# Optimization experiments

Measured on AMD Instinct MI355X. Metric: run time of the kernel, lower is better.

Reference implementation:

```python
import jax, jax.numpy as jnp
import numpy as np

N = 100000   # nodes
E = 3200000  # edges (avg degree 32)
IN = 256     # in_features
OUT = 256    # out_features
L = 4        # n_latent heads
D = OUT // L # per-head emb dim


def setup_inputs() -> dict:
    key = jax.random.key(0)
    ks = jax.random.split(key, 8)
    return {
        "x": jax.random.normal(ks[0], (N, IN), jnp.float32),
        "src": jax.random.randint(ks[1], (E,), 0, N, jnp.int32),
        "dst": jax.random.randint(ks[2], (E,), 0, N, jnp.int32),
        "W_lin": jax.random.normal(ks[3], (IN, OUT), jnp.float32) * (1.0 / np.sqrt(IN)),
        "b_lin": jnp.zeros((OUT,), jnp.float32),
        "att_w": jax.random.normal(ks[4], (L, 2 * OUT), jnp.float32) * (1.0 / np.sqrt(2 * OUT)),
        "att_b": jnp.zeros((L,), jnp.float32),
        "emb_w": jax.random.normal(ks[5], (IN, D), jnp.float32) * (1.0 / np.sqrt(IN)),
        "emb_b": jnp.zeros((D,), jnp.float32),
    }


def reference(x, src, dst, W_lin, b_lin, att_w, att_b, emb_w, emb_b):
    n = x.shape[0]
    h = x @ W_lin + b_lin              # [N, OUT]
    h_em = x @ emb_w + emb_b           # [N, D]
    out_dim = h.shape[1]
    # concat-linear att(cat(h[src], h[dst])) decomposed into separable per-node scores
    a_src = att_w[:, :out_dim]         # [L, OUT]
    a_dst = att_w[:, out_dim:]         # [L, OUT]
    s_src = h @ a_src.T                # [N, L]
    s_dst = h @ a_dst.T                # [N, L]
    # per-edge sigmoid score for all latent heads at once
    e_ob = jax.nn.sigmoid(s_src[src] + s_dst[dst] + att_b)  # [E, L]
    # sparse softmax over edges grouped by source node (FactorGCN sp_softmax)
    ev = jnp.exp(e_ob - jnp.max(e_ob, axis=0, keepdims=True))
    denom = jax.ops.segment_sum(ev, src, num_segments=n)    # [N, L]
    attn = ev / denom[src]                                   # [E, L]
    # sp_matmul: out[src] += attn * h_em[dst], per latent head, then concat
    h_em_dst = h_em[dst]                                     # [E, D]
    heads = [
        jax.ops.segment_sum(attn[:, l:l + 1] * h_em_dst, src, num_segments=n)
        for l in range(att_w.shape[0])
    ]
    return jnp.concatenate(heads, axis=-1)                   # [N, OUT]
```

## Files before the change

### kernel.cpp

```cpp
#include <hip/hip_runtime.h>

#define N_NODES 100000
#define E_EDGES 3200000

#define BSHIFT 7
#define BWIDTH 128
#define NBUCKETS 782
#define BCAP 5120
#define NB1 200
#define CHUNK1 16000

#define WCT_STRIDE 264
#define WCT_ELEMS (80 * WCT_STRIDE)

#define N_TILES (N_NODES / 16)
#define ROW_BLOCKS 768


typedef __attribute__((ext_vector_type(8))) short short8;
typedef __attribute__((ext_vector_type(4))) float f32x4;

__device__ __forceinline__ unsigned short f2bf(float f) {
    unsigned u = __float_as_uint(f);
    return (unsigned short)((u + 0x7FFFu + ((u >> 16) & 1u)) >> 16);
}

__global__ __launch_bounds__(1024) void prep_kernel(
    const float* __restrict__ W_lin, const float* __restrict__ b_lin,
    const float* __restrict__ att_w, const float* __restrict__ emb_w,
    unsigned short* __restrict__ Wct, float* __restrict__ off8,
    const int* __restrict__ src, const int* __restrict__ dst,
    int* __restrict__ gcur, int* __restrict__ pairs) {
    __shared__ int h[NBUCKETS];
    if (blockIdx.x < 64) {
        if (threadIdx.x >= 256) return;
        const int wave = threadIdx.x >> 6, lane = threadIdx.x & 63;
        const int k = blockIdx.x * 4 + wave;
        float4 wv = *(const float4*)(W_lin + k * 256 + lane * 4);
        float acc[8];
#pragma unroll
        for (int j = 0; j < 8; ++j) {
            int l = j & 3, part = j >> 2;
            float4 av = *(const float4*)(att_w + l * 512 + part * 256 + lane * 4);
            acc[j] = wv.x * av.x + wv.y * av.y + wv.z * av.z + wv.w * av.w;
        }
#pragma unroll
        for (int j = 0; j < 8; ++j) {
            float v = acc[j];
#pragma unroll
            for (int off = 32; off >= 1; off >>= 1) v += __shfl_xor(v, off);
            acc[j] = v;
        }
        if (lane < 8) {
            float v = acc[0];
#pragma unroll
            for (int j = 1; j < 8; ++j) if (lane == j) v = acc[j];
            Wct[(64 + lane) * WCT_STRIDE + k] = f2bf(v);
        }
        Wct[lane * WCT_STRIDE + k] = f2bf(emb_w[k * 64 + lane]);
        if (lane < 8) Wct[(72 + lane) * WCT_STRIDE + k] = 0;
        if (k < 8) {
            int l = k & 3, part = k >> 2;
            float4 av = *(const float4*)(att_w + l * 512 + part * 256 + lane * 4);
            float4 bv = *(const float4*)(b_lin + lane * 4);
            float p = bv.x * av.x + bv.y * av.y + bv.z * av.z + bv.w * av.w;
#pragma unroll
            for (int off = 32; off >= 1; off >>= 1) p += __shfl_xor(p, off);
            if (lane == 0) off8[k] = p;
        }
    } else {
        const int pb = blockIdx.x - 64;
        for (int i = threadIdx.x; i < NBUCKETS; i += 1024) h[i] = 0;
        __syncthreads();
        const int base = pb * CHUNK1;
        for (int i = threadIdx.x; i < CHUNK1; i += 1024)
            atomicAdd(&h[src[base + i] >> BSHIFT], 1);
        __syncthreads();
        for (int b = threadIdx.x; b < NBUCKETS; b += 1024) {
            int c = h[b];
            h[b] = c ? atomicAdd(&gcur[b], c) : 0;
        }
        __syncthreads();
        for (int i = threadIdx.x; i < CHUNK1; i += 1024) {
            int s = src[base + i];
            int b = s >> BSHIFT;
            int pos = atomicAdd(&h[b], 1);
            pairs[b * BCAP + pos] = ((s & (BWIDTH - 1)) << 20) | dst[base + i];
        }
    }
}

__global__ __launch_bounds__(256) void mid_kernel(
    const float* __restrict__ x, const unsigned short* __restrict__ Wct,
    const float* __restrict__ off8, const float* __restrict__ att_b,
    const float* __restrict__ emb_b,
    unsigned short* __restrict__ hem, float* __restrict__ s8,
    unsigned short* __restrict__ sdq,
    const int* __restrict__ gcur, const int* __restrict__ pairs,
    int* __restrict__ sdst, int* __restrict__ rowptr,
    int* __restrict__ rowcnt) {
    __shared__ unsigned short Wl[WCT_ELEMS];
    int* h = (int*)Wl;
    const int bid = blockIdx.x;
    const bool is_row = (bid < 2 * ROW_BLOCKS) && ((bid & 1) == 0);
    if (is_row) {
        const int rid = bid >> 1;
        const int tid = threadIdx.x;
        for (int i = tid; i < WCT_ELEMS / 8; i += 256)
            ((uint4*)Wl)[i] = ((const uint4*)Wct)[i];
        __syncthreads();
        const int wave = tid >> 6, lane = tid & 63;
        const int r = lane & 15, g = lane >> 4;
        const int gw = rid * 4 + wave, nw = ROW_BLOCKS * 4;
        for (int tile = gw; tile < N_TILES; tile += nw) {
            const int row0 = tile * 16;
            const float* xr = x + (size_t)(row0 + r) * 256 + g * 8;
            f32x4 acc[5];
#pragma unroll
            for (int n = 0; n < 5; ++n) acc[n] = (f32x4){0.f, 0.f, 0.f, 0.f};
            for (int kk = 0; kk < 8; ++kk) {
                float4 xa = *(const float4*)(xr + kk * 32);
                float4 xb = *(const float4*)(xr + kk * 32 + 4);
                short8 a;
                a[0] = (short)f2bf(xa.x); a[1] = (short)f2bf(xa.y);
                a[2] = (short)f2bf(xa.z); a[3] = (short)f2bf(xa.w);
                a[4] = (short)f2bf(xb.x); a[5] = (short)f2bf(xb.y);
                a[6] = (short)f2bf(xb.z); a[7] = (short)f2bf(xb.w);
                const int bk = kk * 32 + g * 8;
#pragma unroll
                for (int n = 0; n < 5; ++n) {
                    short8 b = *(const short8*)(&Wl[(16 * n + r) * WCT_STRIDE + bk]);
                    acc[n] = __builtin_amdgcn_mfma_f32_16x16x32_bf16(a, b, acc[n],
                                                                     0, 0, 0);
                }
            }
#pragma unroll
            for (int q = 0; q < 4; ++q) {
                const int orow = row0 + g * 4 + q;
                unsigned e0 = f2bf(acc[0][q] + emb_b[r]);
                unsigned e1 = f2bf(acc[1][q] + emb_b[16 + r]);
                unsigned e2 = f2bf(acc[2][q] + emb_b[32 + r]);
                unsigned e3 = f2bf(acc[3][q] + emb_b[48 + r]);
                uint2 hv;
                hv.x = e0 | (e1 << 16);
                hv.y = e2 | (e3 << 16);
                *(uint2*)(hem + (size_t)orow * 64 + r * 4) = hv;
                if (r < 8) {
                    const float sv =
                        acc[4][q] + off8[r] + (r < 4 ? att_b[r] : 0.f);
                    s8[(size_t)orow * 8 + r] = sv;
                    if (r >= 4)
                        sdq[(size_t)orow * 4 + (r - 4)] = f2bf(sv);
                }
            }
        }
    } else {
        const int b = (bid < 2 * ROW_BLOCKS) ? (bid >> 1)
                                             : (ROW_BLOCKS + bid - 2 * ROW_BLOCKS);
        const int t = threadIdx.x;
        const int beg = b * BCAP;
        const int end = beg + gcur[b];
        if (t < BWIDTH) h[t] = 0;
        __syncthreads();
        for (int i = beg + t; i < end; i += 256)
            atomicAdd(&h[pairs[i] >> 20], 1);
        __syncthreads();
        const int s0 = b << BSHIFT;
        if (t < BWIDTH && s0 + t < N_NODES) rowcnt[s0 + t] = h[t];
        __syncthreads();
        if (t == 0) {
            int run = 0;
            for (int i = 0; i < BWIDTH; ++i) { int c = h[i]; h[i] = run; run += c; }
        }
        __syncthreads();
        if (t < BWIDTH && s0 + t < N_NODES) rowptr[s0 + t] = beg + h[t];
        __syncthreads();
        for (int i = beg + t; i < end; i += 256) {
            int p = pairs[i];
            int pos = beg + atomicAdd(&h[p >> 20], 1);
            sdst[pos] = p & 0xFFFFF;
        }
    }
}

template <int MASKED>
__device__ __forceinline__ void node_batch(
    const int* __restrict__ sdst, const unsigned short* __restrict__ sdq,
    const unsigned short* __restrict__ hem, const float2* lut,
    int base, int m, int g, unsigned ru4, int r3, float ssr,
    const short8& bones,
    f32x4& acc0, f32x4& acc1, f32x4& acc2, f32x4& acc3, f32x4& accd) {
    unsigned dj[8];
#pragma unroll
    for (int j = 0; j < 8; ++j) {
        int e = 4 * j + g;
        if (MASKED) e = min(e, m - 1);
        dj[j] = (unsigned)sdst[(unsigned)(base + e)];
    }
    unsigned short sq[8];
    uint2 hv[8];
#pragma unroll
    for (int j = 0; j < 8; ++j) {
        sq[j] = sdq[dj[j] * 4u + (unsigned)r3];
        hv[j] = *(const uint2*)(hem + dj[j] * 64u + ru4);
    }
    short8 a, b0, b1, b2, b3;
#pragma unroll
    for (int j = 0; j < 8; ++j) {
        const float sd = __uint_as_float((unsigned)sq[j] << 16);
        float t = ssr + sd;
        t = fminf(fmaxf(t, -8.0f), 7.96875f);
        const float u = (t + 8.0f) * 32.0f;
        const float fi = truncf(u);
        const float fr = u - fi;
        const float2 e = lut[(int)fi];
        float w = e.x + e.y * fr;
        if (MASKED) w = (4 * j + g < m) ? w : 0.f;
        a[j] = (short)(__float_as_uint(w) >> 16);
        b0[j] = (short)(hv[j].x & 0xFFFFu);
        b1[j] = (short)(hv[j].x >> 16);
        b2[j] = (short)(hv[j].y & 0xFFFFu);
        b3[j] = (short)(hv[j].y >> 16);
    }
    acc0 = __builtin_amdgcn_mfma_f32_16x16x32_bf16(a, b0, acc0, 0, 0, 0);
    acc1 = __builtin_amdgcn_mfma_f32_16x16x32_bf16(a, b1, acc1, 0, 0, 0);
    acc2 = __builtin_amdgcn_mfma_f32_16x16x32_bf16(a, b2, acc2, 0, 0, 0);
    acc3 = __builtin_amdgcn_mfma_f32_16x16x32_bf16(a, b3, acc3, 0, 0, 0);
    accd = __builtin_amdgcn_mfma_f32_16x16x32_bf16(a, bones, accd, 0, 0, 0);
}

__global__ __launch_bounds__(256) void node_kernel(
    const int* __restrict__ rowptr, const int* __restrict__ rowcnt,
    const int* __restrict__ sdst, const float* __restrict__ s8,
    const unsigned short* __restrict__ sdq,
    const unsigned short* __restrict__ hem, float* __restrict__ out) {
    __shared__ float2 lut[512];
    for (int i = threadIdx.x; i < 512; i += 256) {
        const float t0 = -8.0f + i * (1.0f / 32.0f);
        const float t1 = t0 + (1.0f / 32.0f);
        const float w0 = __expf(1.0f / (1.0f + __expf(-t0)));
        const float w1 = __expf(1.0f / (1.0f + __expf(-t1)));
        lut[i] = make_float2(w0, w1 - w0);
    }
    __syncthreads();
    const int lane = threadIdx.x & 63;
    const int r = lane & 15, g = lane >> 4, r3 = r & 3;
    const unsigned ru4 = (unsigned)(r * 4);
    const short8 bones = {16256, 16256, 16256, 16256,
                          16256, 16256, 16256, 16256};
    const int gw = (blockIdx.x * blockDim.x + threadIdx.x) >> 6;
    const int nw = (gridDim.x * blockDim.x) >> 6;
    for (int s = gw; s < N_NODES; s += nw) {
        const int beg = rowptr[s];
        const int deg = rowcnt[s];
        const float ssr = s8[(unsigned)s * 8u + (unsigned)r3];
        f32x4 a0 = {0.f, 0.f, 0.f, 0.f}, a1 = {0.f, 0.f, 0.f, 0.f};
        f32x4 a2 = {0.f, 0.f, 0.f, 0.f}, a3 = {0.f, 0.f, 0.f, 0.f};
        f32x4 ad = {0.f, 0.f, 0.f, 0.f};
        const int nfull = deg >> 5;
        int base = beg;
        for (int f = 0; f < nfull; ++f, base += 32)
            node_batch<0>(sdst, sdq, hem, lut, base, 32, g, ru4, r3, ssr,
                          bones, a0, a1, a2, a3, ad);
        const int m = deg - (base - beg);
        if (m > 0)
            node_batch<1>(sdst, sdq, hem, lut, base, m, g, ru4, r3, ssr,
                          bones, a0, a1, a2, a3, ad);
        const float i0 = ad[0] > 0.f ? 1.f / ad[0] : 0.f;
        const float i1 = ad[1] > 0.f ? 1.f / ad[1] : 0.f;
        const float i2 = ad[2] > 0.f ? 1.f / ad[2] : 0.f;
        const float i3 = ad[3] > 0.f ? 1.f / ad[3] : 0.f;
        f32x4 av = a0;
        if (g == 1) av = a1;
        if (g == 2) av = a2;
        if (g == 3) av = a3;
        float* o = out + (size_t)s * 256 + g * 16 + r;
        o[0]   = av[0] * i0;
        o[64]  = av[1] * i1;
        o[128] = av[2] * i2;
        o[192] = av[3] * i3;
    }
}

extern "C" void kernel_launch(void* const* d_in, const int* in_sizes, int n_in,
                              void* d_out, int out_size, void* d_ws, size_t ws_size,
                              hipStream_t stream) {
    const float* x     = (const float*)d_in[0];
    const int*   src   = (const int*)d_in[1];
    const int*   dst   = (const int*)d_in[2];
    const float* W_lin = (const float*)d_in[3];
    const float* b_lin = (const float*)d_in[4];
    const float* att_w = (const float*)d_in[5];
    const float* att_b = (const float*)d_in[6];
    const float* emb_w = (const float*)d_in[7];
    const float* emb_b = (const float*)d_in[8];
    float* out = (float*)d_out;
    float* ws  = (float*)d_ws;

    unsigned short* hem = (unsigned short*)ws;
    float* s8     = ws + 3200000;
    unsigned short* Wct = (unsigned short*)(ws + 4000000);
    float* off8   = ws + 4010560;
    int*   rowptr = (int*)(ws + 4010568);
    int*   rowcnt = (int*)(ws + 4110568);
    int*   gcur   = (int*)(ws + 4210568);
    unsigned short* sdq = (unsigned short*)(ws + 4211368);
    int*   pairs  = (int*)(ws + 4411368);
    int*   sdst   = (int*)(ws + 8415208);

    hipMemsetAsync(gcur, 0, 800 * sizeof(int), stream);

    prep_kernel<<<64 + NB1, 1024, 0, stream>>>(W_lin, b_lin, att_w, emb_w,
                                               Wct, off8, src, dst, gcur,
                                               pairs);
    mid_kernel<<<2 * ROW_BLOCKS + (NBUCKETS - ROW_BLOCKS), 256, 0, stream>>>(
        x, Wct, off8, att_b, emb_b, hem, s8, sdq, gcur, pairs, sdst, rowptr,
        rowcnt);
    node_kernel<<<4096, 256, 0, stream>>>(rowptr, rowcnt, sdst, s8, sdq, hem,
                                          out);
}
```

Before: 199.1 us.

## Co-schedule edge partitioning with node GEMM, split bucket sort into own kernel

Splits the former prep kernel so the weight-fusion step runs alone. The edge-partition (histogram and scatter) blocks now share a launch with the x·W GEMM row blocks, which use 1024-thread blocks. The per-bucket counting sort moves to a separate kernel. The aim is to overlap the memory-bound edge partitioning with the GEMM instead of running it in the first launch, at the cost of one extra kernel launch and a different GEMM block shape.

Measured after the change: 255.1 us. 1.28x slower.

```diff
diff --git a/kernel.cpp b/kernel.cpp
--- a/kernel.cpp
+++ b/kernel.cpp
@@ -14,7 +14,7 @@
 #define WCT_ELEMS (80 * WCT_STRIDE)
 
 #define N_TILES (N_NODES / 16)
-#define ROW_BLOCKS 768
+#define ROW2_BLOCKS 192
 
 
 typedef __attribute__((ext_vector_type(8))) short short8;
@@ -25,51 +25,58 @@
     return (unsigned short)((u + 0x7FFFu + ((u >> 16) & 1u)) >> 16);
 }
 
-__global__ __launch_bounds__(1024) void prep_kernel(
+__global__ __launch_bounds__(256) void fuse_kernel(
     const float* __restrict__ W_lin, const float* __restrict__ b_lin,
     const float* __restrict__ att_w, const float* __restrict__ emb_w,
-    unsigned short* __restrict__ Wct, float* __restrict__ off8,
+    unsigned short* __restrict__ Wct, float* __restrict__ off8) {
+    const int wave = threadIdx.x >> 6, lane = threadIdx.x & 63;
+    const int k = blockIdx.x * 4 + wave;
+    float4 wv = *(const float4*)(W_lin + k * 256 + lane * 4);
+    float acc[8];
+#pragma unroll
+    for (int j = 0; j < 8; ++j) {
+        int l = j & 3, part = j >> 2;
+        float4 av = *(const float4*)(att_w + l * 512 + part * 256 + lane * 4);
+        acc[j] = wv.x * av.x + wv.y * av.y + wv.z * av.z + wv.w * av.w;
+    }
+#pragma unroll
+    for (int j = 0; j < 8; ++j) {
+        float v = acc[j];
+#pragma unroll
+        for (int off = 32; off >= 1; off >>= 1) v += __shfl_xor(v, off);
+        acc[j] = v;
+    }
+    if (lane < 8) {
+        float v = acc[0];
+#pragma unroll
+        for (int j = 1; j < 8; ++j) if (lane == j) v = acc[j];
+        Wct[(64 + lane) * WCT_STRIDE + k] = f2bf(v);
+    }
+    Wct[lane * WCT_STRIDE + k] = f2bf(emb_w[k * 64 + lane]);
+    if (lane < 8) Wct[(72 + lane) * WCT_STRIDE + k] = 0;
+    if (k < 8) {
+        int l = k & 3, part = k >> 2;
+        float4 av = *(const float4*)(att_w + l * 512 + part * 256 + lane * 4);
+        float4 bv = *(const float4*)(b_lin + lane * 4);
+        float p = bv.x * av.x + bv.y * av.y + bv.z * av.z + bv.w * av.w;
+#pragma unroll
+        for (int off = 32; off >= 1; off >>= 1) p += __shfl_xor(p, off);
+        if (lane == 0) off8[k] = p;
+    }
+}
+
+__global__ __launch_bounds__(1024) void partrow_kernel(
     const int* __restrict__ src, const int* __restrict__ dst,
-    int* __restrict__ gcur, int* __restrict__ pairs) {
-    __shared__ int h[NBUCKETS];
-    if (blockIdx.x < 64) {
-        if (threadIdx.x >= 256) return;
-        const int wave = threadIdx.x >> 6, lane = threadIdx.x & 63;
-        const int k = blockIdx.x * 4 + wave;
-        float4 wv = *(const float4*)(W_lin + k * 256 + lane * 4);
-        float acc[8];
-#pragma unroll
-        for (int j = 0; j < 8; ++j) {
-            int l = j & 3, part = j >> 2;
-            float4 av = *(const float4*)(att_w + l * 512 + part * 256 + lane * 4);
-            acc[j] = wv.x * av.x + wv.y * av.y + wv.z * av.z + wv.w * av.w;
-        }
-#pragma unroll
-        for (int j = 0; j < 8; ++j) {
-            float v = acc[j];
-#pragma unroll
-            for (int off = 32; off >= 1; off >>= 1) v += __shfl_xor(v, off);
-            acc[j] = v;
-        }
-        if (lane < 8) {
-            float v = acc[0];
-#pragma unroll
-            for (int j = 1; j < 8; ++j) if (lane == j) v = acc[j];
-            Wct[(64 + lane) * WCT_STRIDE + k] = f2bf(v);
-        }
-        Wct[lane * WCT_STRIDE + k] = f2bf(emb_w[k * 64 + lane]);
-        if (lane < 8) Wct[(72 + lane) * WCT_STRIDE + k] = 0;
-        if (k < 8) {
-            int l = k & 3, part = k >> 2;
-            float4 av = *(const float4*)(att_w + l * 512 + part * 256 + lane * 4);
-            float4 bv = *(const float4*)(b_lin + lane * 4);
-            float p = bv.x * av.x + bv.y * av.y + bv.z * av.z + bv.w * av.w;
-#pragma unroll
-            for (int off = 32; off >= 1; off >>= 1) p += __shfl_xor(p, off);
-            if (lane == 0) off8[k] = p;
-        }
-    } else {
-        const int pb = blockIdx.x - 64;
+    int* __restrict__ gcur, int* __restrict__ pairs,
+    const float* __restrict__ x, const unsigned short* __restrict__ Wct,
+    const float* __restrict__ off8, const float* __restrict__ att_b,
+    const float* __restrict__ emb_b,
+    unsigned short* __restrict__ hem, float* __restrict__ s8,
+    unsigned short* __restrict__ sdq) {
+    __shared__ unsigned short Wl[WCT_ELEMS];
+    int* h = (int*)Wl;
+    if (blockIdx.x < NB1) {
+        const int pb = blockIdx.x;
         for (int i = threadIdx.x; i < NBUCKETS; i += 1024) h[i] = 0;
         __syncthreads();
         const int base = pb * CHUNK1;
@@ -87,31 +94,15 @@
             int pos = atomicAdd(&h[b], 1);
             pairs[b * BCAP + pos] = ((s & (BWIDTH - 1)) << 20) | dst[base + i];
         }
-    }
-}
-
-__global__ __launch_bounds__(256) void mid_kernel(
-    const float* __restrict__ x, const unsigned short* __restrict__ Wct,
-    const float* __restrict__ off8, const float* __restrict__ att_b,
-    const float* __restrict__ emb_b,
-    unsigned short* __restrict__ hem, float* __restrict__ s8,
-    unsigned short* __restrict__ sdq,
-    const int* __restrict__ gcur, const int* __restrict__ pairs,
-    int* __restrict__ sdst, int* __restrict__ rowptr,
-    int* __restrict__ rowcnt) {
-    __shared__ unsigned short Wl[WCT_ELEMS];
-    int* h = (int*)Wl;
-    const int bid = blockIdx.x;
-    const bool is_row = (bid < 2 * ROW_BLOCKS) && ((bid & 1) == 0);
-    if (is_row) {
-        const int rid = bid >> 1;
+    } else {
+        const int rid = blockIdx.x - NB1;
         const int tid = threadIdx.x;
-        for (int i = tid; i < WCT_ELEMS / 8; i += 256)
+        for (int i = tid; i < WCT_ELEMS / 8; i += 1024)
             ((uint4*)Wl)[i] = ((const uint4*)Wct)[i];
         __syncthreads();
         const int wave = tid >> 6, lane = tid & 63;
         const int r = lane & 15, g = lane >> 4;
-        const int gw = rid * 4 + wave, nw = ROW_BLOCKS * 4;
+        const int gw = rid * 16 + wave, nw = ROW2_BLOCKS * 16;
         for (int tile = gw; tile < N_TILES; tile += nw) {
             const int row0 = tile * 16;
             const float* xr = x + (size_t)(row0 + r) * 256 + g * 8;
@@ -154,32 +145,36 @@
                 }
             }
         }
-    } else {
-        const int b = (bid < 2 * ROW_BLOCKS) ? (bid >> 1)
-                                             : (ROW_BLOCKS + bid - 2 * ROW_BLOCKS);
-        const int t = threadIdx.x;
-        const int beg = b * BCAP;
-        const int end = beg + gcur[b];
-        if (t < BWIDTH) h[t] = 0;
-        __syncthreads();
-        for (int i = beg + t; i < end; i += 256)
-            atomicAdd(&h[pairs[i] >> 20], 1);
-        __syncthreads();
-        const int s0 = b << BSHIFT;
-        if (t < BWIDTH && s0 + t < N_NODES) rowcnt[s0 + t] = h[t];
-        __syncthreads();
-        if (t == 0) {
-            int run = 0;
-            for (int i = 0; i < BWIDTH; ++i) { int c = h[i]; h[i] = run; run += c; }
-        }
-        __syncthreads();
-        if (t < BWIDTH && s0 + t < N_NODES) rowptr[s0 + t] = beg + h[t];
-        __syncthreads();
-        for (int i = beg + t; i < end; i += 256) {
-            int p = pairs[i];
-            int pos = beg + atomicAdd(&h[p >> 20], 1);
-            sdst[pos] = p & 0xFFFFF;
-        }
+    }
+}
+
+__global__ __launch_bounds__(256) void bsort_kernel(
+    const int* __restrict__ gcur, const int* __restrict__ pairs,
+    int* __restrict__ sdst, int* __restrict__ rowptr,
+    int* __restrict__ rowcnt) {
+    __shared__ int h[BWIDTH];
+    const int b = blockIdx.x, t = threadIdx.x;
+    const int beg = b * BCAP;
+    const int end = beg + gcur[b];
+    if (t < BWIDTH) h[t] = 0;
+    __syncthreads();
+    for (int i = beg + t; i < end; i += 256)
+        atomicAdd(&h[pairs[i] >> 20], 1);
+    __syncthreads();
+    const int s0 = b << BSHIFT;
+    if (t < BWIDTH && s0 + t < N_NODES) rowcnt[s0 + t] = h[t];
+    __syncthreads();
+    if (t == 0) {
+        int run = 0;
+        for (int i = 0; i < BWIDTH; ++i) { int c = h[i]; h[i] = run; run += c; }
+    }
+    __syncthreads();
+    if (t < BWIDTH && s0 + t < N_NODES) rowptr[s0 + t] = beg + h[t];
+    __syncthreads();
+    for (int i = beg + t; i < end; i += 256) {
+        int p = pairs[i];
+        int pos = beg + atomicAdd(&h[p >> 20], 1);
+        sdst[pos] = p & 0xFFFFF;
     }
 }
 
@@ -310,12 +305,11 @@
 
     hipMemsetAsync(gcur, 0, 800 * sizeof(int), stream);
 
-    prep_kernel<<<64 + NB1, 1024, 0, stream>>>(W_lin, b_lin, att_w, emb_w,
-                                               Wct, off8, src, dst, gcur,
-                                               pairs);
-    mid_kernel<<<2 * ROW_BLOCKS + (NBUCKETS - ROW_BLOCKS), 256, 0, stream>>>(
-        x, Wct, off8, att_b, emb_b, hem, s8, sdq, gcur, pairs, sdst, rowptr,
-        rowcnt);
+    fuse_kernel<<<64, 256, 0, stream>>>(W_lin, b_lin, att_w, emb_w, Wct, off8);
+    partrow_kernel<<<NB1 + ROW2_BLOCKS, 1024, 0, stream>>>(
+        src, dst, gcur, pairs, x, Wct, off8, att_b, emb_b, hem, s8, sdq);
+    bsort_kernel<<<NBUCKETS, 256, 0, stream>>>(gcur, pairs, sdst, rowptr,
+                                               rowcnt);
     node_kernel<<<4096, 256, 0, stream>>>(rowptr, rowcnt, sdst, s8, sdq, hem,
                                           out);
 }
```
